# Optimization experiments

Hardware: AMD Instinct MI355X
Metric: run time of the kernel (lower is better)

The kernel has to match this reference:

```python
import jax, jax.numpy as jnp
import numpy as np

T, B, D, H, L = 64, 512, 1536, 1024, 4
DISCOUNT = 0.997
LAM = 0.95


def setup_inputs() -> dict:
    key = jax.random.key(0)
    ks = jax.random.split(key, 3 + L + 1)
    inp = {
        'feat': jax.random.normal(ks[0], (T, B, D), dtype=jnp.float32),
        'reward': jax.random.normal(ks[1], (T - 1, B), dtype=jnp.float32),
        'cont': jnp.ones((T, B), dtype=jnp.float32),
    }
    scale = 0.02
    dims = [D] + [H] * L
    for i in range(L):
        inp[f'W{i}'] = jax.random.normal(ks[3 + i], (dims[i], dims[i + 1]), dtype=jnp.float32) * scale
        inp[f'b{i}'] = jnp.zeros((dims[i + 1],), dtype=jnp.float32)
    inp['Wo'] = jax.random.normal(ks[3 + L], (H,), dtype=jnp.float32) * scale
    inp['bo'] = jnp.zeros((), dtype=jnp.float32)
    return inp


def reference(feat, reward, cont, W0, b0, W1, b1, W2, b2, W3, b3, Wo, bo):
    # Value-net MLP (mean of critic dist): [T, B, D] -> [T, B]
    h = feat
    for W, b in ((W0, b0), (W1, b1), (W2, b2), (W3, b3)):
        h = jax.nn.silu(h @ W + b)
    value = h @ Wo + bo  # [T, B]

    disc = cont[1:] * DISCOUNT                      # [T-1, B]
    deltas = reward + disc * value[1:] - value[:-1]  # [T-1, B]

    # GAE: adv_t = delta_t + disc_t * lambda * adv_{t+1}, adv_T = 0
    def step(adv_next, xs):
        delta, dl = xs
        adv = delta + dl * adv_next
        return adv, adv

    _, advs = jax.lax.scan(step, jnp.zeros_like(value[0]),
                           (deltas, disc * LAM), reverse=True)
    ret = advs + value[:-1]   # lambda-return target, [T-1, B]
    baseline = value[:-1]
    return ret, baseline
```

## Files before the change

kernel.cpp:

```cpp
#include <hip/hip_runtime.h>
#include <hip/hip_bf16.h>

#define T_DIM 64
#define B_DIM 512
#define D_DIM 1536
#define H_DIM 1024
#define M_DIM (T_DIM * B_DIM)
#define DISCOUNT 0.997f
#define LAM 0.95f

#define BM 256
#define BN 256
#define BK 32
#define TILES_M (M_DIM / BM)
#define TILES_N (H_DIM / BN)
#define N_XCD 8

typedef __bf16 bf16x8 __attribute__((ext_vector_type(8)));
typedef float  f32x4  __attribute__((ext_vector_type(4)));

__device__ __forceinline__ void async_load16(const void* g, void* l) {
    __builtin_amdgcn_global_load_lds(
        (const __attribute__((address_space(1))) void*)g,
        (__attribute__((address_space(3))) void*)l,
        16, 0, 0);
}

__device__ __forceinline__ unsigned short f2bf_raw(float f) {
    __hip_bfloat16 h = __float2bfloat16(f);
    return *reinterpret_cast<unsigned short*>(&h);
}

__global__ __launch_bounds__(256) void cvt_bf16_kernel(
    const float* __restrict__ x, __hip_bfloat16* __restrict__ y, long n4) {
    long i = (long)blockIdx.x * blockDim.x + threadIdx.x;
    if (i >= n4) return;
    float4 v = reinterpret_cast<const float4*>(x)[i];
    ushort4 o;
    o.x = f2bf_raw(v.x);
    o.y = f2bf_raw(v.y);
    o.z = f2bf_raw(v.z);
    o.w = f2bf_raw(v.w);
    reinterpret_cast<ushort4*>(y)[i] = o;
}

__global__ __launch_bounds__(256) void transpose_cvt_all_kernel(
    const float* __restrict__ W0, const float* __restrict__ W1,
    const float* __restrict__ W2, const float* __restrict__ W3,
    __hip_bfloat16* __restrict__ T0, __hip_bfloat16* __restrict__ T1,
    __hip_bfloat16* __restrict__ T2, __hip_bfloat16* __restrict__ T3) {
    __shared__ float tile[32][33];
    int z = blockIdx.z;
    const float* W;
    __hip_bfloat16* Tt;
    int K;
    if (z == 0)      { W = W0; Tt = T0; K = D_DIM; }
    else if (z == 1) { W = W1; Tt = T1; K = H_DIM; }
    else if (z == 2) { W = W2; Tt = T2; K = H_DIM; }
    else             { W = W3; Tt = T3; K = H_DIM; }
    int k0 = blockIdx.x * 32, n0 = blockIdx.y * 32;
    if (k0 >= K) return;
    int tx = threadIdx.x, ty = threadIdx.y;
    #pragma unroll
    for (int r = ty; r < 32; r += 8)
        tile[r][tx] = W[(size_t)(k0 + r) * H_DIM + n0 + tx];
    __syncthreads();
    #pragma unroll
    for (int r = ty; r < 32; r += 8)
        Tt[(size_t)(n0 + r) * K + k0 + tx] = __float2bfloat16(tile[tx][r]);
}

__global__ __launch_bounds__(512, 2) void gemm_silu_kernel(
    const __hip_bfloat16* __restrict__ A,
    const __hip_bfloat16* __restrict__ Bt,
    const float* __restrict__ bias,
    __hip_bfloat16* __restrict__ C,
    int K) {

    __shared__ alignas(16) __hip_bfloat16 lds[65536];

    const int tid  = threadIdx.x;
    const int wave = tid >> 6;
    const int lane = tid & 63;
    const int quad = lane >> 4;
    const int r16  = lane & 15;
    const int wm   = wave & 1;
    const int wn   = wave >> 1;

    const int l     = blockIdx.x;
    const int xcd   = l & (N_XCD - 1);
    const int local = l >> 3;
    const int tn    = local & (TILES_N - 1);
    const int tm    = (xcd << 4) | (local >> 2);
    const int m0 = tm * BM;
    const int n0 = tn * BN;

    const int rsub = lane >> 2;
    const int cgrp = lane & 3;
    const int scol = ((cgrp ^ ((rsub >> 1) & 3)) << 3);
    const __hip_bfloat16* gA = A  + (size_t)(m0 + wave * 32 + rsub) * K + scol;
    const __hip_bfloat16* gB = Bt + (size_t)(n0 + wave * 32 + rsub) * K + scol;
    const int ldsOf0 = (wave * 32) * 32;
    const int ldsOf1 = (wave * 32 + 16) * 32;

    const int swz    = ((quad ^ ((r16 >> 1) & 3)) << 3);
    const int rdoffA = (wm * 128 + r16) * 32 + swz;
    const int rdoffB = (wn * 64  + r16) * 32 + swz;

    f32x4 acc[8][4];
    #pragma unroll
    for (int i = 0; i < 8; ++i)
        #pragma unroll
        for (int j = 0; j < 4; ++j)
            acc[i][j] = (f32x4){0.f, 0.f, 0.f, 0.f};

#define STAGE(tt) do { \
        const int sbb = (tt) & 3; \
        __hip_bfloat16* Ab_ = &lds[sbb * 8192]; \
        __hip_bfloat16* Bb_ = &lds[32768 + sbb * 8192]; \
        const size_t ko_ = (size_t)(tt) * BK; \
        async_load16(gA + ko_,                  Ab_ + ldsOf0); \
        async_load16(gA + ko_ + (size_t)16 * K, Ab_ + ldsOf1); \
        async_load16(gB + ko_,                  Bb_ + ldsOf0); \
        async_load16(gB + ko_ + (size_t)16 * K, Bb_ + ldsOf1); \
    } while (0)

#define RD_A(i) (*reinterpret_cast<const bf16x8*>(Ab + rdoffA + (i) * 512))
#define RD_B(j) (*reinterpret_cast<const bf16x8*>(Bb + rdoffB + (j) * 512))

#define MM(i, areg) do { \
        acc[i][0] = __builtin_amdgcn_mfma_f32_16x16x32_bf16(b0, areg, acc[i][0], 0, 0, 0); \
        acc[i][1] = __builtin_amdgcn_mfma_f32_16x16x32_bf16(b1, areg, acc[i][1], 0, 0, 0); \
        acc[i][2] = __builtin_amdgcn_mfma_f32_16x16x32_bf16(b2, areg, acc[i][2], 0, 0, 0); \
        acc[i][3] = __builtin_amdgcn_mfma_f32_16x16x32_bf16(b3, areg, acc[i][3], 0, 0, 0); \
    } while (0)

#define BODY(t, VMCNT, DOSTAGE) do { \
        asm volatile("s_waitcnt vmcnt(" #VMCNT ")" ::: "memory"); \
        __builtin_amdgcn_s_barrier(); \
        __builtin_amdgcn_sched_barrier(0); \
        if (DOSTAGE) STAGE((t) + 3); \
        const int bb = (t) & 3; \
        const __hip_bfloat16* Ab = &lds[bb * 8192]; \
        const __hip_bfloat16* Bb = &lds[32768 + bb * 8192]; \
        bf16x8 b0 = RD_B(0), b1 = RD_B(1), b2 = RD_B(2), b3 = RD_B(3); \
        bf16x8 a0 = RD_A(0), a1 = RD_A(1), a2 = RD_A(2), a3 = RD_A(3); \
        __builtin_amdgcn_s_setprio(1); MM(0, a0); MM(1, a1); __builtin_amdgcn_s_setprio(0); \
        __builtin_amdgcn_sched_barrier(0); \
        a0 = RD_A(4); a1 = RD_A(5); \
        __builtin_amdgcn_s_setprio(1); MM(2, a2); MM(3, a3); __builtin_amdgcn_s_setprio(0); \
        __builtin_amdgcn_sched_barrier(0); \
        a2 = RD_A(6); a3 = RD_A(7); \
        __builtin_amdgcn_s_setprio(1); MM(4, a0); MM(5, a1); __builtin_amdgcn_s_setprio(0); \
        __builtin_amdgcn_sched_barrier(0); \
        __builtin_amdgcn_s_setprio(1); MM(6, a2); MM(7, a3); __builtin_amdgcn_s_setprio(0); \
    } while (0)

    STAGE(0); STAGE(1); STAGE(2);

    const int NT = K / BK;
    for (int t = 0; t < NT - 2; ++t)
        BODY(t, 8, (t + 3 < NT));
    BODY(NT - 2, 4, false);
    BODY(NT - 1, 0, false);

#undef STAGE
#undef RD_A
#undef RD_B
#undef MM
#undef BODY

    #pragma unroll
    for (int j = 0; j < 4; ++j) {
        const int c0 = n0 + wn * 64 + j * 16 + quad * 4;
        const float4 b4 = *reinterpret_cast<const float4*>(&bias[c0]);
        const float* bp = reinterpret_cast<const float*>(&b4);
        #pragma unroll
        for (int i = 0; i < 8; ++i) {
            const int row = m0 + wm * 128 + i * 16 + r16;
            ushort4 o;
            unsigned short* op = reinterpret_cast<unsigned short*>(&o);
            #pragma unroll
            for (int rr = 0; rr < 4; ++rr) {
                const float v = acc[i][j][rr] + bp[rr];
                const float s = v / (1.f + __expf(-v));
                op[rr] = f2bf_raw(s);
            }
            *reinterpret_cast<ushort4*>(&C[(size_t)row * H_DIM + c0]) = o;
        }
    }
}

__global__ __launch_bounds__(256) void gemv_value_kernel(
    const __hip_bfloat16* __restrict__ H,
    const float* __restrict__ Wo,
    const float* __restrict__ bo_p,
    float* __restrict__ value, int M) {
    int wave = threadIdx.x >> 6, lane = threadIdx.x & 63;
    int row = blockIdx.x * 4 + wave;
    if (row >= M) return;
    const __hip_bfloat16* hrow = H + (size_t)row * H_DIM;
    float sum = 0.f;
    #pragma unroll
    for (int half = 0; half < 2; ++half) {
        int col = half * 512 + lane * 8;
        uint4 raw = *reinterpret_cast<const uint4*>(hrow + col);
        const __hip_bfloat16* hp = reinterpret_cast<const __hip_bfloat16*>(&raw);
        #pragma unroll
        for (int e = 0; e < 8; ++e)
            sum += __bfloat162float(hp[e]) * Wo[col + e];
    }
    #pragma unroll
    for (int off = 32; off > 0; off >>= 1)
        sum += __shfl_down(sum, off, 64);
    if (lane == 0) value[row] = sum + bo_p[0];
}

__global__ __launch_bounds__(64) void gae_kernel(
    const float* __restrict__ value,
    const float* __restrict__ reward,
    const float* __restrict__ cont,
    float* __restrict__ out) {
    int b = blockIdx.x * blockDim.x + threadIdx.x;
    if (b >= B_DIM) return;
    float adv = 0.f;
    float v_next = value[(T_DIM - 1) * B_DIM + b];
    for (int t = T_DIM - 2; t >= 0; --t) {
        float v_t  = value[t * B_DIM + b];
        float disc = cont[(t + 1) * B_DIM + b] * DISCOUNT;
        float delta = reward[t * B_DIM + b] + disc * v_next - v_t;
        adv = delta + disc * LAM * adv;
        out[t * B_DIM + b] = adv + v_t;
        out[(T_DIM - 1) * B_DIM + t * B_DIM + b] = v_t;
        v_next = v_t;
    }
}

extern "C" void kernel_launch(void* const* d_in, const int* in_sizes, int n_in,
                              void* d_out, int out_size, void* d_ws, size_t ws_size,
                              hipStream_t stream) {
    const float* feat   = (const float*)d_in[0];
    const float* reward = (const float*)d_in[1];
    const float* cont   = (const float*)d_in[2];
    const float* W[4]   = {(const float*)d_in[3], (const float*)d_in[5],
                           (const float*)d_in[7], (const float*)d_in[9]};
    const float* bias[4] = {(const float*)d_in[4], (const float*)d_in[6],
                            (const float*)d_in[8], (const float*)d_in[10]};
    const float* Wo = (const float*)d_in[11];
    const float* bo = (const float*)d_in[12];
    float* out = (float*)d_out;

    char* ws = (char*)d_ws;
    __hip_bfloat16* Xb = (__hip_bfloat16*)ws; ws += (size_t)M_DIM * D_DIM * 2;
    __hip_bfloat16* Ha = (__hip_bfloat16*)ws; ws += (size_t)M_DIM * H_DIM * 2;
    __hip_bfloat16* Hb = (__hip_bfloat16*)ws; ws += (size_t)M_DIM * H_DIM * 2;
    __hip_bfloat16* Wt0 = (__hip_bfloat16*)ws; ws += (size_t)H_DIM * D_DIM * 2;
    __hip_bfloat16* Wt1 = (__hip_bfloat16*)ws; ws += (size_t)H_DIM * H_DIM * 2;
    __hip_bfloat16* Wt2 = (__hip_bfloat16*)ws; ws += (size_t)H_DIM * H_DIM * 2;
    __hip_bfloat16* Wt3 = (__hip_bfloat16*)ws; ws += (size_t)H_DIM * H_DIM * 2;
    float* value = (float*)ws; ws += (size_t)M_DIM * 4;

    long n4 = (long)M_DIM * D_DIM / 4;
    cvt_bf16_kernel<<<(int)((n4 + 255) / 256), 256, 0, stream>>>(feat, Xb, n4);

    transpose_cvt_all_kernel<<<dim3(D_DIM / 32, H_DIM / 32, 4), dim3(32, 8), 0, stream>>>(
        W[0], W[1], W[2], W[3], Wt0, Wt1, Wt2, Wt3);

    const int nblocks = TILES_M * TILES_N;
    gemm_silu_kernel<<<nblocks, 512, 0, stream>>>(Xb, Wt0, bias[0], Ha, D_DIM);
    gemm_silu_kernel<<<nblocks, 512, 0, stream>>>(Ha, Wt1, bias[1], Hb, H_DIM);
    gemm_silu_kernel<<<nblocks, 512, 0, stream>>>(Hb, Wt2, bias[2], Ha, H_DIM);
    gemm_silu_kernel<<<nblocks, 512, 0, stream>>>(Ha, Wt3, bias[3], Hb, H_DIM);

    gemv_value_kernel<<<M_DIM / 4, 256, 0, stream>>>(Hb, Wo, bo, value, M_DIM);

    gae_kernel<<<8, 64, 0, stream>>>(value, reward, cont, out);
}
```

Before: 686.8 us.

## Split GEMM K-step into four barrier-synced phases interleaving loads and MFMA quadrants

Restructures the GEMM main-loop body into four phases, each issuing one async global-to-LDS load, a subset of LDS fragment reads, a workgroup barrier plus lgkmcnt wait, and a quadrant of MFMAs. The goal is to spread the global loads and LDS reads across the compute so memory traffic overlaps the matrix work, in the style of ping-pong scheduling. It adds three extra barriers per K-step and rereads the B low fragments, which may add sync stalls and LDS traffic.

```diff
diff --git a/kernel.cpp b/kernel.cpp
--- a/kernel.cpp
+++ b/kernel.cpp
@@ -114,49 +114,69 @@
         for (int j = 0; j < 4; ++j)
             acc[i][j] = (f32x4){0.f, 0.f, 0.f, 0.f};
 
-#define STAGE(tt) do { \
-        const int sbb = (tt) & 3; \
-        __hip_bfloat16* Ab_ = &lds[sbb * 8192]; \
-        __hip_bfloat16* Bb_ = &lds[32768 + sbb * 8192]; \
+#define STAGE1(tt, w) do { \
+        const int sbb_ = (tt) & 3; \
         const size_t ko_ = (size_t)(tt) * BK; \
-        async_load16(gA + ko_,                  Ab_ + ldsOf0); \
-        async_load16(gA + ko_ + (size_t)16 * K, Ab_ + ldsOf1); \
-        async_load16(gB + ko_,                  Bb_ + ldsOf0); \
-        async_load16(gB + ko_ + (size_t)16 * K, Bb_ + ldsOf1); \
+        if ((w) == 0) async_load16(gA + ko_,                  &lds[sbb_ * 8192] + ldsOf0); \
+        if ((w) == 1) async_load16(gA + ko_ + (size_t)16 * K, &lds[sbb_ * 8192] + ldsOf1); \
+        if ((w) == 2) async_load16(gB + ko_,                  &lds[32768 + sbb_ * 8192] + ldsOf0); \
+        if ((w) == 3) async_load16(gB + ko_ + (size_t)16 * K, &lds[32768 + sbb_ * 8192] + ldsOf1); \
     } while (0)
 
 #define RD_A(i) (*reinterpret_cast<const bf16x8*>(Ab + rdoffA + (i) * 512))
 #define RD_B(j) (*reinterpret_cast<const bf16x8*>(Bb + rdoffB + (j) * 512))
 
-#define MM(i, areg) do { \
-        acc[i][0] = __builtin_amdgcn_mfma_f32_16x16x32_bf16(b0, areg, acc[i][0], 0, 0, 0); \
-        acc[i][1] = __builtin_amdgcn_mfma_f32_16x16x32_bf16(b1, areg, acc[i][1], 0, 0, 0); \
-        acc[i][2] = __builtin_amdgcn_mfma_f32_16x16x32_bf16(b2, areg, acc[i][2], 0, 0, 0); \
-        acc[i][3] = __builtin_amdgcn_mfma_f32_16x16x32_bf16(b3, areg, acc[i][3], 0, 0, 0); \
+#define MMQ(mq, nq, AF, BF) do { \
+        _Pragma("unroll") \
+        for (int ii = 0; ii < 4; ++ii) { \
+            acc[(mq)*4+ii][(nq)*2+0] = __builtin_amdgcn_mfma_f32_16x16x32_bf16( \
+                BF[0], AF[ii], acc[(mq)*4+ii][(nq)*2+0], 0, 0, 0); \
+            acc[(mq)*4+ii][(nq)*2+1] = __builtin_amdgcn_mfma_f32_16x16x32_bf16( \
+                BF[1], AF[ii], acc[(mq)*4+ii][(nq)*2+1], 0, 0, 0); \
+        } \
+    } while (0)
+
+#define PHASE_SYNC() do { \
+        __builtin_amdgcn_s_barrier(); \
+        asm volatile("s_waitcnt lgkmcnt(0)" ::: "memory"); \
+        __builtin_amdgcn_sched_barrier(0); \
     } while (0)
 
 #define BODY(t, VMCNT, DOSTAGE) do { \
         asm volatile("s_waitcnt vmcnt(" #VMCNT ")" ::: "memory"); \
         __builtin_amdgcn_s_barrier(); \
         __builtin_amdgcn_sched_barrier(0); \
-        if (DOSTAGE) STAGE((t) + 3); \
         const int bb = (t) & 3; \
         const __hip_bfloat16* Ab = &lds[bb * 8192]; \
         const __hip_bfloat16* Bb = &lds[32768 + bb * 8192]; \
-        bf16x8 b0 = RD_B(0), b1 = RD_B(1), b2 = RD_B(2), b3 = RD_B(3); \
-        bf16x8 a0 = RD_A(0), a1 = RD_A(1), a2 = RD_A(2), a3 = RD_A(3); \
-        __builtin_amdgcn_s_setprio(1); MM(0, a0); MM(1, a1); __builtin_amdgcn_s_setprio(0); \
-        __builtin_amdgcn_sched_barrier(0); \
-        a0 = RD_A(4); a1 = RD_A(5); \
-        __builtin_amdgcn_s_setprio(1); MM(2, a2); MM(3, a3); __builtin_amdgcn_s_setprio(0); \
-        __builtin_amdgcn_sched_barrier(0); \
-        a2 = RD_A(6); a3 = RD_A(7); \
-        __builtin_amdgcn_s_setprio(1); MM(4, a0); MM(5, a1); __builtin_amdgcn_s_setprio(0); \
-        __builtin_amdgcn_sched_barrier(0); \
-        __builtin_amdgcn_s_setprio(1); MM(6, a2); MM(7, a3); __builtin_amdgcn_s_setprio(0); \
-    } while (0)
-
-    STAGE(0); STAGE(1); STAGE(2);
+        bf16x8 aLo[4], aHi[4], bLo[2], bHi[2]; \
+         \
+        if (DOSTAGE) STAGE1((t) + 3, 0); \
+        bLo[0] = RD_B(0); bLo[1] = RD_B(1); \
+        aLo[0] = RD_A(0); aLo[1] = RD_A(1); aLo[2] = RD_A(2); aLo[3] = RD_A(3); \
+        PHASE_SYNC(); \
+        __builtin_amdgcn_s_setprio(1); MMQ(0, 0, aLo, bLo); __builtin_amdgcn_s_setprio(0); \
+         \
+        if (DOSTAGE) STAGE1((t) + 3, 1); \
+        bHi[0] = RD_B(2); bHi[1] = RD_B(3); \
+        PHASE_SYNC(); \
+        __builtin_amdgcn_s_setprio(1); MMQ(0, 1, aLo, bHi); __builtin_amdgcn_s_setprio(0); \
+         \
+        if (DOSTAGE) STAGE1((t) + 3, 2); \
+        aHi[0] = RD_A(4); aHi[1] = RD_A(5); aHi[2] = RD_A(6); aHi[3] = RD_A(7); \
+        PHASE_SYNC(); \
+        __builtin_amdgcn_s_setprio(1); MMQ(1, 1, aHi, bHi); __builtin_amdgcn_s_setprio(0); \
+         \
+        if (DOSTAGE) STAGE1((t) + 3, 3); \
+        bLo[0] = RD_B(0); bLo[1] = RD_B(1); \
+        PHASE_SYNC(); \
+        __builtin_amdgcn_s_setprio(1); MMQ(1, 0, aHi, bLo); __builtin_amdgcn_s_setprio(0); \
+    } while (0)
+
+    #pragma unroll
+    for (int pt = 0; pt < 3; ++pt) {
+        STAGE1(pt, 0); STAGE1(pt, 1); STAGE1(pt, 2); STAGE1(pt, 3);
+    }
 
     const int NT = K / BK;
     for (int t = 0; t < NT - 2; ++t)
@@ -164,10 +184,11 @@
     BODY(NT - 2, 4, false);
     BODY(NT - 1, 0, false);
 
-#undef STAGE
+#undef STAGE1
 #undef RD_A
 #undef RD_B
-#undef MM
+#undef MMQ
+#undef PHASE_SYNC
 #undef BODY
 
     #pragma unroll
```

Measured after the change: 702.0 us. 1.02x slower.

## Fuse value GEMV into last GEMM epilogue and simplify MFMA scheduling

Applied to the files above, without the earlier changes.

The last SiLU GEMM now takes the Wo dot product in its epilogue instead of writing the hidden activations. Each block reduces partial row sums through shuffles and LDS, then atomically adds them into a value buffer that the conversion kernel zeroes first. The bias bo moves into the GAE kernel, and the separate GEMV kernel goes away, avoiding a 64 MB write and reread. The hand-interleaved LDS-read/MFMA schedule with setprio and sched_barrier is also replaced by plain unrolled loops. That may change instruction scheduling for all four GEMMs, and the float atomics make the summation order nondeterministic.

```diff
diff --git a/kernel.cpp b/kernel.cpp
--- a/kernel.cpp
+++ b/kernel.cpp
@@ -32,9 +32,12 @@
 }
 
 __global__ __launch_bounds__(256) void cvt_bf16_kernel(
-    const float* __restrict__ x, __hip_bfloat16* __restrict__ y, long n4) {
+    const float* __restrict__ x, __hip_bfloat16* __restrict__ y, long n4,
+    float* __restrict__ value) {
     long i = (long)blockIdx.x * blockDim.x + threadIdx.x;
     if (i >= n4) return;
+    if (i < M_DIM / 4)
+        reinterpret_cast<float4*>(value)[i] = (float4){0.f, 0.f, 0.f, 0.f};
     float4 v = reinterpret_cast<const float4*>(x)[i];
     ushort4 o;
     o.x = f2bf_raw(v.x);
@@ -75,7 +78,9 @@
     const __hip_bfloat16* __restrict__ Bt,
     const float* __restrict__ bias,
     __hip_bfloat16* __restrict__ C,
-    int K) {
+    int K,
+    const float* __restrict__ Wo,
+    float* __restrict__ value) {
 
     __shared__ alignas(16) __hip_bfloat16 lds[65536];
 
@@ -128,32 +133,24 @@
 #define RD_A(i) (*reinterpret_cast<const bf16x8*>(Ab + rdoffA + (i) * 512))
 #define RD_B(j) (*reinterpret_cast<const bf16x8*>(Bb + rdoffB + (j) * 512))
 
-#define MM(i, areg) do { \
-        acc[i][0] = __builtin_amdgcn_mfma_f32_16x16x32_bf16(b0, areg, acc[i][0], 0, 0, 0); \
-        acc[i][1] = __builtin_amdgcn_mfma_f32_16x16x32_bf16(b1, areg, acc[i][1], 0, 0, 0); \
-        acc[i][2] = __builtin_amdgcn_mfma_f32_16x16x32_bf16(b2, areg, acc[i][2], 0, 0, 0); \
-        acc[i][3] = __builtin_amdgcn_mfma_f32_16x16x32_bf16(b3, areg, acc[i][3], 0, 0, 0); \
-    } while (0)
-
 #define BODY(t, VMCNT, DOSTAGE) do { \
         asm volatile("s_waitcnt vmcnt(" #VMCNT ")" ::: "memory"); \
         __builtin_amdgcn_s_barrier(); \
-        __builtin_amdgcn_sched_barrier(0); \
         if (DOSTAGE) STAGE((t) + 3); \
         const int bb = (t) & 3; \
         const __hip_bfloat16* Ab = &lds[bb * 8192]; \
         const __hip_bfloat16* Bb = &lds[32768 + bb * 8192]; \
-        bf16x8 b0 = RD_B(0), b1 = RD_B(1), b2 = RD_B(2), b3 = RD_B(3); \
-        bf16x8 a0 = RD_A(0), a1 = RD_A(1), a2 = RD_A(2), a3 = RD_A(3); \
-        __builtin_amdgcn_s_setprio(1); MM(0, a0); MM(1, a1); __builtin_amdgcn_s_setprio(0); \
-        __builtin_amdgcn_sched_barrier(0); \
-        a0 = RD_A(4); a1 = RD_A(5); \
-        __builtin_amdgcn_s_setprio(1); MM(2, a2); MM(3, a3); __builtin_amdgcn_s_setprio(0); \
-        __builtin_amdgcn_sched_barrier(0); \
-        a2 = RD_A(6); a3 = RD_A(7); \
-        __builtin_amdgcn_s_setprio(1); MM(4, a0); MM(5, a1); __builtin_amdgcn_s_setprio(0); \
-        __builtin_amdgcn_sched_barrier(0); \
-        __builtin_amdgcn_s_setprio(1); MM(6, a2); MM(7, a3); __builtin_amdgcn_s_setprio(0); \
+        bf16x8 bfr[4], af[8]; \
+        _Pragma("unroll") \
+        for (int j = 0; j < 4; ++j) bfr[j] = RD_B(j); \
+        _Pragma("unroll") \
+        for (int i = 0; i < 8; ++i) af[i] = RD_A(i); \
+        _Pragma("unroll") \
+        for (int i = 0; i < 8; ++i) \
+            _Pragma("unroll") \
+            for (int j = 0; j < 4; ++j) \
+                acc[i][j] = __builtin_amdgcn_mfma_f32_16x16x32_bf16( \
+                    bfr[j], af[i], acc[i][j], 0, 0, 0); \
     } while (0)
 
     STAGE(0); STAGE(1); STAGE(2);
@@ -167,66 +164,80 @@
 #undef STAGE
 #undef RD_A
 #undef RD_B
-#undef MM
 #undef BODY
 
-    #pragma unroll
-    for (int j = 0; j < 4; ++j) {
-        const int c0 = n0 + wn * 64 + j * 16 + quad * 4;
-        const float4 b4 = *reinterpret_cast<const float4*>(&bias[c0]);
-        const float* bp = reinterpret_cast<const float*>(&b4);
+    if (value == nullptr) {
+        #pragma unroll
+        for (int j = 0; j < 4; ++j) {
+            const int c0 = n0 + wn * 64 + j * 16 + quad * 4;
+            const float4 b4 = *reinterpret_cast<const float4*>(&bias[c0]);
+            const float* bp = reinterpret_cast<const float*>(&b4);
+            #pragma unroll
+            for (int i = 0; i < 8; ++i) {
+                const int row = m0 + wm * 128 + i * 16 + r16;
+                ushort4 o;
+                unsigned short* op = reinterpret_cast<unsigned short*>(&o);
+                #pragma unroll
+                for (int rr = 0; rr < 4; ++rr) {
+                    const float v = acc[i][j][rr] + bp[rr];
+                    const float s = v / (1.f + __expf(-v));
+                    op[rr] = f2bf_raw(s);
+                }
+                *reinterpret_cast<ushort4*>(&C[(size_t)row * H_DIM + c0]) = o;
+            }
+        }
+    } else {
+        float part[8];
+        #pragma unroll
+        for (int i = 0; i < 8; ++i) part[i] = 0.f;
+        #pragma unroll
+        for (int j = 0; j < 4; ++j) {
+            const int c0 = n0 + wn * 64 + j * 16 + quad * 4;
+            const float4 b4 = *reinterpret_cast<const float4*>(&bias[c0]);
+            const float4 w4 = *reinterpret_cast<const float4*>(&Wo[c0]);
+            const float* bp = reinterpret_cast<const float*>(&b4);
+            const float* wp = reinterpret_cast<const float*>(&w4);
+            #pragma unroll
+            for (int i = 0; i < 8; ++i) {
+                #pragma unroll
+                for (int rr = 0; rr < 4; ++rr) {
+                    const float v = acc[i][j][rr] + bp[rr];
+                    const float s = v / (1.f + __expf(-v));
+                    part[i] += s * wp[rr];
+                }
+            }
+        }
+        __syncthreads();
+        float* lds_v = reinterpret_cast<float*>(lds);
         #pragma unroll
         for (int i = 0; i < 8; ++i) {
-            const int row = m0 + wm * 128 + i * 16 + r16;
-            ushort4 o;
-            unsigned short* op = reinterpret_cast<unsigned short*>(&o);
-            #pragma unroll
-            for (int rr = 0; rr < 4; ++rr) {
-                const float v = acc[i][j][rr] + bp[rr];
-                const float s = v / (1.f + __expf(-v));
-                op[rr] = f2bf_raw(s);
-            }
-            *reinterpret_cast<ushort4*>(&C[(size_t)row * H_DIM + c0]) = o;
+            float p = part[i];
+            p += __shfl_xor(p, 16, 64);
+            p += __shfl_xor(p, 32, 64);
+            if (quad == 0)
+                lds_v[(wm * 128 + i * 16 + r16) * 4 + wn] = p;
+        }
+        __syncthreads();
+        if (tid < 256) {
+            const float* row = &lds_v[tid * 4];
+            atomicAdd(&value[m0 + tid], row[0] + row[1] + row[2] + row[3]);
         }
     }
-}
-
-__global__ __launch_bounds__(256) void gemv_value_kernel(
-    const __hip_bfloat16* __restrict__ H,
-    const float* __restrict__ Wo,
-    const float* __restrict__ bo_p,
-    float* __restrict__ value, int M) {
-    int wave = threadIdx.x >> 6, lane = threadIdx.x & 63;
-    int row = blockIdx.x * 4 + wave;
-    if (row >= M) return;
-    const __hip_bfloat16* hrow = H + (size_t)row * H_DIM;
-    float sum = 0.f;
-    #pragma unroll
-    for (int half = 0; half < 2; ++half) {
-        int col = half * 512 + lane * 8;
-        uint4 raw = *reinterpret_cast<const uint4*>(hrow + col);
-        const __hip_bfloat16* hp = reinterpret_cast<const __hip_bfloat16*>(&raw);
-        #pragma unroll
-        for (int e = 0; e < 8; ++e)
-            sum += __bfloat162float(hp[e]) * Wo[col + e];
-    }
-    #pragma unroll
-    for (int off = 32; off > 0; off >>= 1)
-        sum += __shfl_down(sum, off, 64);
-    if (lane == 0) value[row] = sum + bo_p[0];
 }
 
 __global__ __launch_bounds__(64) void gae_kernel(
     const float* __restrict__ value,
     const float* __restrict__ reward,
     const float* __restrict__ cont,
+    const float* __restrict__ bo_p,
     float* __restrict__ out) {
     int b = blockIdx.x * blockDim.x + threadIdx.x;
     if (b >= B_DIM) return;
+    const float bo = bo_p[0];
     float adv = 0.f;
-    float v_next = value[(T_DIM - 1) * B_DIM + b];
+    float v_next = value[(T_DIM - 1) * B_DIM + b] + bo;
     for (int t = T_DIM - 2; t >= 0; --t) {
-        float v_t  = value[t * B_DIM + b];
+        float v_t  = value[t * B_DIM + b] + bo;
         float disc = cont[(t + 1) * B_DIM + b] * DISCOUNT;
         float delta = reward[t * B_DIM + b] + disc * v_next - v_t;
         adv = delta + disc * LAM * adv;
@@ -261,18 +272,20 @@
     float* value = (float*)ws; ws += (size_t)M_DIM * 4;
 
     long n4 = (long)M_DIM * D_DIM / 4;
-    cvt_bf16_kernel<<<(int)((n4 + 255) / 256), 256, 0, stream>>>(feat, Xb, n4);
+    cvt_bf16_kernel<<<(int)((n4 + 255) / 256), 256, 0, stream>>>(feat, Xb, n4, value);
 
     transpose_cvt_all_kernel<<<dim3(D_DIM / 32, H_DIM / 32, 4), dim3(32, 8), 0, stream>>>(
         W[0], W[1], W[2], W[3], Wt0, Wt1, Wt2, Wt3);
 
     const int nblocks = TILES_M * TILES_N;
-    gemm_silu_kernel<<<nblocks, 512, 0, stream>>>(Xb, Wt0, bias[0], Ha, D_DIM);
-    gemm_silu_kernel<<<nblocks, 512, 0, stream>>>(Ha, Wt1, bias[1], Hb, H_DIM);
-    gemm_silu_kernel<<<nblocks, 512, 0, stream>>>(Hb, Wt2, bias[2], Ha, H_DIM);
-    gemm_silu_kernel<<<nblocks, 512, 0, stream>>>(Ha, Wt3, bias[3], Hb, H_DIM);
-
-    gemv_value_kernel<<<M_DIM / 4, 256, 0, stream>>>(Hb, Wo, bo, value, M_DIM);
-
-    gae_kernel<<<8, 64, 0, stream>>>(value, reward, cont, out);
-}
+    gemm_silu_kernel<<<nblocks, 512, 0, stream>>>(Xb, Wt0, bias[0], Ha, D_DIM,
+                                                  nullptr, nullptr);
+    gemm_silu_kernel<<<nblocks, 512, 0, stream>>>(Ha, Wt1, bias[1], Hb, H_DIM,
+                                                  nullptr, nullptr);
+    gemm_silu_kernel<<<nblocks, 512, 0, stream>>>(Hb, Wt2, bias[2], Ha, H_DIM,
+                                                  nullptr, nullptr);
+    gemm_silu_kernel<<<nblocks, 512, 0, stream>>>(Ha, Wt3, bias[3], Hb, H_DIM,
+                                                  Wo, value);
+
+    gae_kernel<<<8, 64, 0, stream>>>(value, reward, cont, bo, out);
+}
```

Result: slower. 717.9 us (+4.5%).
